# Optimization experiments

Measured on AMD Instinct MI355X. Metric: run time of the kernel, lower is better.

The kernel has to match this reference:

```python
import jax, jax.numpy as jnp
import numpy as np

D_MODEL = 512
D_STATE = 16
D_CONV = 4
EXPAND = 2
DT_RANK = 32
D_INNER = EXPAND * D_MODEL  # 1024


def setup_inputs() -> dict:
    key = jax.random.key(0)
    ks = jax.random.split(key, 8)
    s = 0.02
    return {
        "x": jax.random.normal(ks[0], (4, 2048, D_MODEL), jnp.float32),
        "ln1_w": jnp.ones((D_MODEL,), jnp.float32),
        "ln1_b": jnp.zeros((D_MODEL,), jnp.float32),
        "ln2_w": jnp.ones((D_MODEL,), jnp.float32),
        "ln2_b": jnp.zeros((D_MODEL,), jnp.float32),
        "W_in": jax.random.normal(ks[1], (D_MODEL, 2 * D_INNER), jnp.float32) * s,
        "conv_w": jax.random.normal(ks[2], (D_INNER, D_CONV), jnp.float32) * s,
        "conv_b": jnp.zeros((D_INNER,), jnp.float32),
        "W_xproj": jax.random.normal(ks[3], (D_INNER, DT_RANK + 2 * D_STATE), jnp.float32) * s,
        "W_dt": jax.random.normal(ks[4], (DT_RANK, D_INNER), jnp.float32) * s,
        "b_dt": jnp.full((D_INNER,), -4.6, jnp.float32),  # softplus(b_dt) ~ 0.01 init
        "A_log": jnp.log(jnp.broadcast_to(
            jnp.arange(1, D_STATE + 1, dtype=jnp.float32), (D_INNER, D_STATE))),
        "D_param": jnp.ones((D_INNER,), jnp.float32),
        "W_out": jax.random.normal(ks[5], (D_INNER, D_MODEL), jnp.float32) * s,
    }


def _layernorm(x, w, b, eps=1e-5):
    m = x.mean(-1, keepdims=True)
    v = ((x - m) ** 2).mean(-1, keepdims=True)
    return (x - m) / jnp.sqrt(v + eps) * w + b


def _selective_scan(x, W_in, conv_w, conv_b, W_xproj, W_dt, b_dt, A_log, D_param, W_out):
    B, L, _ = x.shape
    # input projection -> ssm branch u and gate branch z
    xz = x @ W_in                               # [B, L, 2E]
    u, z = jnp.split(xz, 2, axis=-1)            # each [B, L, E]

    # depthwise causal conv over L
    uc = jax.lax.conv_general_dilated(
        u.transpose(0, 2, 1),                   # [B, E, L]
        conv_w[:, None, :],                     # [E, 1, K]
        window_strides=(1,),
        padding=[(D_CONV - 1, 0)],
        dimension_numbers=("NCH", "OIH", "NCH"),
        feature_group_count=D_INNER,
    ).transpose(0, 2, 1)                        # [B, L, E]
    u = jax.nn.silu(uc + conv_b)

    # data-dependent SSM parameters
    x_dbl = u @ W_xproj                         # [B, L, R+2N]
    dt_r = x_dbl[..., :DT_RANK]
    Bm = x_dbl[..., DT_RANK:DT_RANK + D_STATE]  # [B, L, N]
    Cm = x_dbl[..., DT_RANK + D_STATE:]         # [B, L, N]
    dt = jax.nn.softplus(dt_r @ W_dt + b_dt)    # [B, L, E]
    A = -jnp.exp(A_log)                         # [E, N]

    def step(h, inp):
        dt_t, B_t, C_t, u_t = inp               # [B,E], [B,N], [B,N], [B,E]
        dA = jnp.exp(dt_t[:, :, None] * A)      # [B, E, N]
        h = dA * h + (dt_t * u_t)[:, :, None] * B_t[:, None, :]
        y = jnp.einsum("ben,bn->be", h, C_t)
        return h, y

    h0 = jnp.zeros((B, D_INNER, D_STATE), x.dtype)
    _, ys = jax.lax.scan(
        step, h0,
        (dt.transpose(1, 0, 2), Bm.transpose(1, 0, 2),
         Cm.transpose(1, 0, 2), u.transpose(1, 0, 2)))
    y = ys.transpose(1, 0, 2) + u * D_param     # skip via D
    y = y * jax.nn.silu(z)                      # gating
    return y @ W_out                            # [B, L, D]


def reference(x, ln1_w, ln1_b, ln2_w, ln2_b, W_in, conv_w, conv_b,
              W_xproj, W_dt, b_dt, A_log, D_param, W_out):
    residual = x
    h = _layernorm(x, ln1_w, ln1_b)
    h = _selective_scan(h, W_in, conv_w, conv_b, W_xproj, W_dt, b_dt,
                        A_log, D_param, W_out)
    return _layernorm(residual + h, ln2_w, ln2_b)
```

## Files before the change

kernel.cpp:

```cpp
#include <hip/hip_runtime.h>
#include <math.h>

#define BATCH   4
#define SEQ     2048
#define DMODEL  512
#define DINNER  1024
#define DSTATE  16
#define DCONV   4
#define DTRANK  32
#define ROWS    (BATCH*SEQ)

#define NCHUNK  128
#define CHUNK   (SEQ / NCHUNK)
#define NBE     (BATCH*DINNER)

typedef unsigned short u16;
typedef __attribute__((ext_vector_type(8))) u16 u16x8;
typedef __attribute__((ext_vector_type(4))) u16 u16x4;
typedef __attribute__((ext_vector_type(8))) short bf16x8;
typedef __attribute__((ext_vector_type(4))) float f32x4;
typedef __attribute__((ext_vector_type(2))) float f32x2;

__device__ inline float bf2f(u16 v) { return __uint_as_float(((unsigned)v) << 16); }
__device__ inline u16 f2bf(float f) {
    unsigned u = __float_as_uint(f);
    return (u16)((u + 0x7fff + ((u >> 16) & 1)) >> 16);
}
__device__ inline f32x2 fma2(f32x2 a, f32x2 b, f32x2 c) {
    return __builtin_elementwise_fma(a, b, c);
}


__global__ __launch_bounds__(256) void prep_weights(const float* __restrict__ W_in,
                                                    const float* __restrict__ W_out,
                                                    const float* __restrict__ W_xp,
                                                    const float* __restrict__ W_dt,
                                                    const float* __restrict__ cw,
                                                    const float* __restrict__ x,
                                                    const float* __restrict__ ln1_w,
                                                    const float* __restrict__ ln1_b,
                                                    u16* __restrict__ Wt,
                                                    u16* __restrict__ Wot,
                                                    u16* __restrict__ Wxt,
                                                    u16* __restrict__ Wdtt,
                                                    u16* __restrict__ cwT,
                                                    u16* __restrict__ hbf)
{
    const int t = blockIdx.x;
    if (t >= 1648) {
        __shared__ float ls[4], lq[4];
        const int row = (t - 1648) * 2 + (threadIdx.x >> 7);
        const int tid = threadIdx.x & 127;
        const int wv = threadIdx.x >> 6;
        float4 v = ((const float4*)(x + (size_t)row * DMODEL))[tid];
        float s = v.x + v.y + v.z + v.w;
        float q = v.x*v.x + v.y*v.y + v.z*v.z + v.w*v.w;
        #pragma unroll
        for (int o = 32; o > 0; o >>= 1) {
            s += __shfl_down(s, o);
            q += __shfl_down(q, o);
        }
        if ((threadIdx.x & 63) == 0) { ls[wv] = s; lq[wv] = q; }
        __syncthreads();
        const int rb = (threadIdx.x >> 7) * 2;
        float mean = (ls[rb] + ls[rb + 1]) * (1.f / DMODEL);
        float var  = (lq[rb] + lq[rb + 1]) * (1.f / DMODEL) - mean * mean;
        float inv  = rsqrtf(var + 1e-5f);
        float4 wv4 = ((const float4*)ln1_w)[tid];
        float4 bv = ((const float4*)ln1_b)[tid];
        u16x4 o4;
        o4.x = f2bf((v.x - mean) * inv * wv4.x + bv.x);
        o4.y = f2bf((v.y - mean) * inv * wv4.y + bv.y);
        o4.z = f2bf((v.z - mean) * inv * wv4.z + bv.z);
        o4.w = f2bf((v.w - mean) * inv * wv4.w + bv.w);
        ((u16x4*)(hbf + (size_t)row * DMODEL))[tid] = o4;
        return;
    }
    if (t >= 1632) {
        int idx = (t - 1632) * 256 + threadIdx.x;
        int j = idx >> 10, e = idx & (DINNER - 1);
        cwT[idx] = f2bf(cw[e * DCONV + j]);
        return;
    }
    const float* W; u16* Wo; int K, N, tl;
    if (t < 1024)      { W = W_in;  Wo = Wt;   K = 512;  N = 2048; tl = t; }
    else if (t < 1536) { W = W_out; Wo = Wot;  K = 1024; N = 512;  tl = t - 1024; }
    else if (t < 1600) { W = W_xp;  Wo = Wxt;  K = 1024; N = 64;   tl = t - 1536; }
    else               { W = W_dt;  Wo = Wdtt; K = 32;   N = 1024; tl = t - 1600; }
    const int ntx = N / 32;
    const int nb = (tl % ntx) * 32, kb = (tl / ntx) * 32;
    __shared__ float sh[32][33];
    const int xx = threadIdx.x & 31, yy = threadIdx.x >> 5;
    #pragma unroll
    for (int i = 0; i < 32; i += 8)
        sh[yy + i][xx] = W[(size_t)(kb + yy + i) * N + nb + xx];
    __syncthreads();
    #pragma unroll
    for (int i = 0; i < 32; i += 8)
        Wo[(size_t)(nb + yy + i) * K + kb + xx] = f2bf(sh[xx][yy + i]);
}

__global__ __launch_bounds__(128) void ln2_kernel(const float* __restrict__ x,
                                                  const u16* __restrict__ og,
                                                  const float* __restrict__ w,
                                                  const float* __restrict__ bb,
                                                  float* __restrict__ out)
{
    const int row = blockIdx.x;
    const int tid = threadIdx.x;
    float4 v = ((const float4*)(x + (size_t)row * DMODEL))[tid];
    u16x4 r4 = ((const u16x4*)(og + (size_t)row * DMODEL))[tid];
    v.x += bf2f(r4.x); v.y += bf2f(r4.y); v.z += bf2f(r4.z); v.w += bf2f(r4.w);
    float s = v.x + v.y + v.z + v.w;
    float q = v.x*v.x + v.y*v.y + v.z*v.z + v.w*v.w;
    #pragma unroll
    for (int o = 32; o > 0; o >>= 1) {
        s += __shfl_down(s, o);
        q += __shfl_down(q, o);
    }
    __shared__ float ls[2], lq[2];
    if ((tid & 63) == 0) { ls[tid >> 6] = s; lq[tid >> 6] = q; }
    __syncthreads();
    float mean = (ls[0] + ls[1]) * (1.f / DMODEL);
    float var  = (lq[0] + lq[1]) * (1.f / DMODEL) - mean * mean;
    float inv  = rsqrtf(var + 1e-5f);
    float4 wv = ((const float4*)w)[tid];
    float4 bv = ((const float4*)bb)[tid];
    float4 o4;
    o4.x = (v.x - mean) * inv * wv.x + bv.x;
    o4.y = (v.y - mean) * inv * wv.y + bv.y;
    o4.z = (v.z - mean) * inv * wv.z + bv.z;
    o4.w = (v.w - mean) * inv * wv.w + bv.w;
    ((float4*)(out + (size_t)row * DMODEL))[tid] = o4;
}

template<bool BF16OUT>
__global__ __launch_bounds__(256) void gemm_bf16(const u16* __restrict__ A, int lda,
                                                 const u16* __restrict__ Bt, int ldb,
                                                 void* __restrict__ Cout, int ldc, int K)
{
    __shared__ u16 Asm[128 * 32];
    __shared__ u16 Bsm[128 * 32];
    const int tid = threadIdx.x;
    const int wid = tid >> 6, lane = tid & 63;
    const int wm = wid >> 1, wn = wid & 1;
    const int bm = blockIdx.y * 128, bn = blockIdx.x * 128;

    f32x4 acc[4][4];
    #pragma unroll
    for (int m = 0; m < 4; ++m)
        #pragma unroll
        for (int n = 0; n < 4; ++n)
            acc[m][n] = (f32x4)(0.f);

    for (int k0 = 0; k0 < K; k0 += 32) {
        __syncthreads();
        #pragma unroll
        for (int j = 0; j < 2; ++j) {
            int c = (wid * 2 + j) * 64 + lane;
            int row = c >> 2, kp = (c & 3) << 3;
            const u16* ga = A  + (size_t)(bm + row) * lda + k0 + kp;
            const u16* gb = Bt + (size_t)(bn + row) * ldb + k0 + kp;
            __builtin_amdgcn_global_load_lds(
                (const __attribute__((address_space(1))) unsigned int*)ga,
                (__attribute__((address_space(3))) unsigned int*)(Asm + (wid * 2 + j) * 512),
                16, 0, 0);
            __builtin_amdgcn_global_load_lds(
                (const __attribute__((address_space(1))) unsigned int*)gb,
                (__attribute__((address_space(3))) unsigned int*)(Bsm + (wid * 2 + j) * 512),
                16, 0, 0);
        }
        __syncthreads();

        const int rl = lane & 15, kf = (lane >> 4) << 3;
        bf16x8 af[4], bfr[4];
        #pragma unroll
        for (int m = 0; m < 4; ++m)
            af[m] = *(const bf16x8*)&Asm[(wm * 64 + m * 16 + rl) * 32 + kf];
        #pragma unroll
        for (int n = 0; n < 4; ++n)
            bfr[n] = *(const bf16x8*)&Bsm[(wn * 64 + n * 16 + rl) * 32 + kf];
        #pragma unroll
        for (int m = 0; m < 4; ++m)
            #pragma unroll
            for (int n = 0; n < 4; ++n)
                acc[m][n] = __builtin_amdgcn_mfma_f32_16x16x32_bf16(af[m], bfr[n], acc[m][n], 0, 0, 0);
    }

    const int rl = lane & 15, rq = lane >> 4;
    #pragma unroll
    for (int m = 0; m < 4; ++m)
        #pragma unroll
        for (int n = 0; n < 4; ++n) {
            int r0 = bm + wm * 64 + m * 16 + rq * 4;
            int cc = bn + wn * 64 + n * 16 + rl;
            #pragma unroll
            for (int j = 0; j < 4; ++j) {
                if (BF16OUT)
                    ((u16*)Cout)[(size_t)(r0 + j) * ldc + cc] = f2bf(acc[m][n][j]);
                else
                    ((float*)Cout)[(size_t)(r0 + j) * ldc + cc] = acc[m][n][j];
            }
        }
}

__global__ __launch_bounds__(512) void conv_xproj_dt(const u16* __restrict__ xzb,
                                                     const u16* __restrict__ cwT,
                                                     const float* __restrict__ cb,
                                                     const u16* __restrict__ Wxt,
                                                     const u16* __restrict__ Wdtt,
                                                     const float* __restrict__ bdt,
                                                     u16* __restrict__ ucb,
                                                     float* __restrict__ xdbl,
                                                     u16* __restrict__ dty,
                                                     float* __restrict__ dts)
{
    __shared__ u16 uc_lds[16][1032];
    __shared__ float xd0[16][72];
    __shared__ float xd1[16][72];
    const int r16 = blockIdx.x;
    const int row0 = r16 * 16;
    const int cbch = ((r16 & 127) << 2) | (r16 >> 7);
    const int tid = threadIdx.x;
    const int lane = tid & 63, wid = tid >> 6;
    const int rl = lane & 15, hi = lane >> 4;

    #pragma unroll
    for (int i = 0; i < 4; ++i) {
        int task = tid + i * 512;
        int r = task >> 7;
        int e0 = (task & 127) * 8;
        int gr = row0 + r;
        int t = gr & (SEQ - 1);
        float4 cb0 = *(const float4*)&cb[e0];
        float4 cb1 = *(const float4*)&cb[e0 + 4];
        float acc[8] = {cb0.x, cb0.y, cb0.z, cb0.w, cb1.x, cb1.y, cb1.z, cb1.w};
        #pragma unroll
        for (int j = 0; j < 4; ++j) {
            int ts = t - 3 + j;
            if (ts >= 0) {
                u16x8 v = *(const u16x8*)&xzb[(size_t)(gr - 3 + j) * (2 * DINNER) + e0];
                u16x8 w = *(const u16x8*)&cwT[j * DINNER + e0];
                #pragma unroll
                for (int k = 0; k < 8; ++k)
                    acc[k] = fmaf(bf2f(v[k]), bf2f(w[k]), acc[k]);
            }
        }
        u16x8 o;
        #pragma unroll
        for (int k = 0; k < 8; ++k) {
            float sig = 1.f / (1.f + __expf(-acc[k]));
            o[k] = f2bf(acc[k] * sig);
        }
        *(u16x8*)&ucb[(size_t)gr * DINNER + e0] = o;
        *(u16x8*)&uc_lds[r][e0] = o;
    }
    __syncthreads();

    {
        const int tile = wid & 3, khalf = wid >> 2;
        f32x4 acc = (f32x4)(0.f);
        const int kbase = khalf * 512;
        #pragma unroll 4
        for (int kk = 0; kk < 512; kk += 32) {
            int k0 = kbase + kk;
            bf16x8 a = *(const bf16x8*)&uc_lds[rl][k0 + hi * 8];
            bf16x8 b = *(const bf16x8*)&Wxt[(size_t)(tile * 16 + rl) * DINNER + k0 + hi * 8];
            acc = __builtin_amdgcn_mfma_f32_16x16x32_bf16(a, b, acc, 0, 0, 0);
        }
        float (*dst)[72] = khalf ? xd1 : xd0;
        #pragma unroll
        for (int j = 0; j < 4; ++j)
            dst[hi * 4 + j][tile * 16 + rl] = acc[j];
    }
    __syncthreads();
    {
        int idx = tid * 2;
        #pragma unroll
        for (int i = 0; i < 2; ++i, ++idx) {
            int r = idx >> 6, c = idx & 63;
            float v = xd0[r][c] + xd1[r][c];
            xd0[r][c] = v;
            if (c >= DTRANK)
                xdbl[(size_t)(row0 + r) * 64 + c] = v;
        }
    }
    __syncthreads();

    {
        bf16x8 af;
        #pragma unroll
        for (int k = 0; k < 8; ++k)
            af[k] = (short)f2bf(xd0[rl][hi * 8 + k]);
        #pragma unroll
        for (int tile = 0; tile < 8; ++tile) {
            int cc = wid * 128 + tile * 16 + rl;
            bf16x8 bfr = *(const bf16x8*)&Wdtt[(size_t)cc * DTRANK + hi * 8];
            f32x4 acc = __builtin_amdgcn_mfma_f32_16x16x32_bf16(af, bfr, (f32x4)(0.f), 0, 0, 0);
            float bias = bdt[cc];
            float ssum = 0.f;
            #pragma unroll
            for (int j = 0; j < 4; ++j) {
                float v = acc[j] + bias;
                float sp = (v > 20.f) ? v : log1pf(__expf(v));
                u16 spb = f2bf(sp);
                dty[(size_t)(row0 + hi * 4 + j) * DINNER + cc] = spb;
                ssum += bf2f(spb);
            }
            ssum += __shfl_xor(ssum, 16);
            ssum += __shfl_xor(ssum, 32);
            if (hi == 0)
                dts[(size_t)cbch * DINNER + cc] = ssum;
        }
    }
}

__device__ inline void pow_tree16(float q, f32x2 dA2[8])
{
    float q2 = q * q;
    f32x2 q2s = {q2, q2};
    dA2[0] = (f32x2){q, q2};
    dA2[1] = dA2[0] * q2s;
    dA2[2] = dA2[1] * q2s;
    dA2[3] = dA2[2] * q2s;
    float q8 = dA2[3].y;
    f32x2 q8s = {q8, q8};
    dA2[4] = dA2[0] * q8s;
    dA2[5] = dA2[1] * q8s;
    dA2[6] = dA2[2] * q8s;
    dA2[7] = dA2[3] * q8s;
}

__global__ __launch_bounds__(256) void scan_pass1(const u16* __restrict__ dtb,
                                                  const u16* __restrict__ ucb,
                                                  const float* __restrict__ xdbl,
                                                  u16* __restrict__ hfinb)
{
    const int cb = blockIdx.x >> 2;
    const int e = ((blockIdx.x & 3) << 8) + threadIdx.x;
    const int b = cb & 3, c = cb >> 2;
    const int row0 = b * SEQ + c * CHUNK;

    __shared__ float bc[CHUNK][32];
    {
        int idx = threadIdx.x;
        #pragma unroll
        for (int i = 0; i < 2; ++i, idx += 256) {
            int r = idx >> 5, cix = idx & 31;
            bc[r][cix] = xdbl[(size_t)(row0 + r) * 64 + DTRANK + cix];
        }
    }
    __syncthreads();

    const u16* pdt = dtb + (size_t)row0 * DINNER + e;
    const u16* puc = ucb + (size_t)row0 * DINNER + e;

    f32x2 h2[8];
    #pragma unroll
    for (int k = 0; k < 8; ++k) h2[k] = (f32x2){0.f, 0.f};

    #pragma unroll 4
    for (int t = 0; t < CHUNK; ++t) {
        float dtv = bf2f(*pdt);
        float uv  = bf2f(*puc);
        float du  = dtv * uv;
        float q = __expf(-dtv);
        f32x2 dA2[8];
        pow_tree16(q, dA2);
        f32x2 du2 = {du, du};
        const f32x2* pbc = (const f32x2*)bc[t];
        #pragma unroll
        for (int k = 0; k < 8; ++k)
            h2[k] = fma2(dA2[k], h2[k], du2 * pbc[k]);
        pdt += DINNER; puc += DINNER;
    }
    #pragma unroll
    for (int k = 0; k < 8; ++k) {
        size_t si = (size_t)(cb * DSTATE + 2 * k) * DINNER + e;
        hfinb[si] = f2bf(h2[k].x);
        hfinb[si + DINNER] = f2bf(h2[k].y);
    }
}

__global__ __launch_bounds__(256) void scan_pass2(const float* __restrict__ dts,
                                                  u16* __restrict__ hfinb)
{
    int j = blockIdx.x * 256 + threadIdx.x;
    int e = j & (DINNER - 1);
    int n = (j >> 10) & 15;
    int b = j >> 14;
    const float mnp1 = -(float)(n + 1);
    float h = 0.f;
    #pragma unroll 4
    for (int c = 0; c < NCHUNK; ++c) {
        int cb = c * BATCH + b;
        size_t si = (size_t)(cb * DSTATE + n) * DINNER + e;
        float t = bf2f(hfinb[si]);
        hfinb[si] = f2bf(h);
        float P = __expf(mnp1 * dts[(size_t)cb * DINNER + e]);
        h = fmaf(P, h, t);
    }
}

__global__ __launch_bounds__(256) void scan_pass3(const u16* __restrict__ xzb,
                                                  const u16* __restrict__ ucb,
                                                  const float* __restrict__ xdbl,
                                                  const float* __restrict__ Dparam,
                                                  const u16* __restrict__ hinb,
                                                  u16* dty)
{
    const int cb = blockIdx.x >> 2;
    const int e = ((blockIdx.x & 3) << 8) + threadIdx.x;
    const int b = cb & 3, c = cb >> 2;
    const int row0 = b * SEQ + c * CHUNK;

    __shared__ float bc[CHUNK][32];
    {
        int idx = threadIdx.x;
        #pragma unroll
        for (int i = 0; i < 2; ++i, idx += 256) {
            int r = idx >> 5, cix = idx & 31;
            bc[r][cix] = xdbl[(size_t)(row0 + r) * 64 + DTRANK + cix];
        }
    }
    __syncthreads();

    const u16* pz  = xzb + (size_t)row0 * (2 * DINNER) + DINNER + e;
    const u16* puc = ucb + (size_t)row0 * DINNER + e;
    u16* pdty = dty + (size_t)row0 * DINNER + e;

    f32x2 h2[8];
    #pragma unroll
    for (int k = 0; k < 8; ++k) {
        size_t si = (size_t)(cb * DSTATE + 2 * k) * DINNER + e;
        h2[k] = (f32x2){bf2f(hinb[si]), bf2f(hinb[si + DINNER])};
    }
    const float Dv = Dparam[e];

    #pragma unroll 4
    for (int t = 0; t < CHUNK; ++t) {
        float dtv = bf2f(*pdty);
        float zv  = bf2f(*pz);
        float uv  = bf2f(*puc);
        float du  = dtv * uv;
        float q = __expf(-dtv);
        f32x2 dA2[8];
        pow_tree16(q, dA2);
        f32x2 du2 = {du, du};
        f32x2 acc = {0.f, 0.f};
        const f32x2* pbc = (const f32x2*)bc[t];
        #pragma unroll
        for (int k = 0; k < 8; ++k) {
            h2[k] = fma2(dA2[k], h2[k], du2 * pbc[k]);
            acc = fma2(h2[k], pbc[8 + k], acc);
        }
        float y = fmaf(uv, Dv, acc.x + acc.y);
        y *= zv / (1.f + __expf(-zv));
        *pdty = f2bf(y);
        pz += 2 * DINNER; puc += DINNER; pdty += DINNER;
    }
}

extern "C" void kernel_launch(void* const* d_in, const int* in_sizes, int n_in,
                              void* d_out, int out_size, void* d_ws, size_t ws_size,
                              hipStream_t stream)
{
    const float* x       = (const float*)d_in[0];
    const float* ln1_w   = (const float*)d_in[1];
    const float* ln1_b   = (const float*)d_in[2];
    const float* ln2_w   = (const float*)d_in[3];
    const float* ln2_b   = (const float*)d_in[4];
    const float* W_in    = (const float*)d_in[5];
    const float* conv_w  = (const float*)d_in[6];
    const float* conv_b  = (const float*)d_in[7];
    const float* W_xproj = (const float*)d_in[8];
    const float* W_dt    = (const float*)d_in[9];
    const float* b_dt    = (const float*)d_in[10];
    const float* D_param = (const float*)d_in[12];
    const float* W_out   = (const float*)d_in[13];
    float* out = (float*)d_out;
    float* ws  = (float*)d_ws;

    u16*   xzb   = (u16*)ws;
    u16*   ucb   = (u16*)(ws + 8388608);
    float* xdbl  = ws + 12582912;
    u16*   hbf   = (u16*)(ws + 13107200);
    u16*   Wt    = (u16*)(ws + 15204352);
    u16*   Wot   = (u16*)(ws + 15728640);
    u16*   dty   = (u16*)(ws + 15990784);
    float* dts   = ws + 20185088;
    u16*   hfinb = (u16*)(ws + 20709376);
    u16*   ogb   = (u16*)(ws + 24903680);
    u16*   Wxt   = (u16*)(ws + 27000832);
    u16*   cwT   = (u16*)(ws + 27033600);
    u16*   Wdtt  = (u16*)(ws + 27035648);

    prep_weights<<<1648 + ROWS / 2, 256, 0, stream>>>(W_in, W_out, W_xproj, W_dt,
                                                      conv_w, x, ln1_w, ln1_b,
                                                      Wt, Wot, Wxt, Wdtt, cwT, hbf);
    gemm_bf16<true><<<dim3(2048 / 128, ROWS / 128), 256, 0, stream>>>(hbf, 512, Wt, 512, xzb, 2048, 512);
    conv_xproj_dt<<<ROWS / 16, 512, 0, stream>>>(xzb, cwT, conv_b, Wxt, Wdtt, b_dt,
                                                 ucb, xdbl, dty, dts);
    scan_pass1<<<NBE * NCHUNK / 256, 256, 0, stream>>>(dty, ucb, xdbl, hfinb);
    scan_pass2<<<BATCH * DSTATE * DINNER / 256, 256, 0, stream>>>(dts, hfinb);
    scan_pass3<<<NBE * NCHUNK / 256, 256, 0, stream>>>(xzb, ucb, xdbl, D_param, hfinb, dty);
    gemm_bf16<true><<<dim3(512 / 128, ROWS / 128), 256, 0, stream>>>(dty, 1024, Wot, 1024, ogb, 512, 1024);
    ln2_kernel<<<ROWS, 128, 0, stream>>>(x, ogb, ln2_w, ln2_b, out);
}
```

Measured before the change: 183.8 us.

## Fuse chunked scan pass 1 into conv/xproj/dt kernel using LDS-resident tiles

Removes the separate scan_pass1 kernel and runs the per-chunk state accumulation at the end of conv_xproj_dt. The dt and conv outputs for the 16-row chunk stay in LDS, and B comes from the xd0 buffer. This saves one launch and the global re-read of dt, u and B. In exchange, each thread now carries two channels' 16-state recurrences serially, which raises register pressure and adds LDS use (a second 16x1032 buffer). That may lower occupancy of the fused kernel.

```diff
diff --git a/kernel.cpp b/kernel.cpp
--- a/kernel.cpp
+++ b/kernel.cpp
@@ -30,6 +30,22 @@
     return __builtin_elementwise_fma(a, b, c);
 }
 
+
+__device__ inline void pow_tree16(float q, f32x2 dA2[8])
+{
+    float q2 = q * q;
+    f32x2 q2s = {q2, q2};
+    dA2[0] = (f32x2){q, q2};
+    dA2[1] = dA2[0] * q2s;
+    dA2[2] = dA2[1] * q2s;
+    dA2[3] = dA2[2] * q2s;
+    float q8 = dA2[3].y;
+    f32x2 q8s = {q8, q8};
+    dA2[4] = dA2[0] * q8s;
+    dA2[5] = dA2[1] * q8s;
+    dA2[6] = dA2[2] * q8s;
+    dA2[7] = dA2[3] * q8s;
+}
 
 __global__ __launch_bounds__(256) void prep_weights(const float* __restrict__ W_in,
                                                     const float* __restrict__ W_out,
@@ -213,9 +229,11 @@
                                                      u16* __restrict__ ucb,
                                                      float* __restrict__ xdbl,
                                                      u16* __restrict__ dty,
-                                                     float* __restrict__ dts)
+                                                     float* __restrict__ dts,
+                                                     u16* __restrict__ hfinb)
 {
     __shared__ u16 uc_lds[16][1032];
+    __shared__ u16 dt_lds[16][1032];
     __shared__ float xd0[16][72];
     __shared__ float xd1[16][72];
     const int r16 = blockIdx.x;
@@ -305,6 +323,7 @@
                 float sp = (v > 20.f) ? v : log1pf(__expf(v));
                 u16 spb = f2bf(sp);
                 dty[(size_t)(row0 + hi * 4 + j) * DINNER + cc] = spb;
+                dt_lds[hi * 4 + j][cc] = spb;
                 ssum += bf2f(spb);
             }
             ssum += __shfl_xor(ssum, 16);
@@ -313,72 +332,45 @@
                 dts[(size_t)cbch * DINNER + cc] = ssum;
         }
     }
-}
-
-__device__ inline void pow_tree16(float q, f32x2 dA2[8])
-{
-    float q2 = q * q;
-    f32x2 q2s = {q2, q2};
-    dA2[0] = (f32x2){q, q2};
-    dA2[1] = dA2[0] * q2s;
-    dA2[2] = dA2[1] * q2s;
-    dA2[3] = dA2[2] * q2s;
-    float q8 = dA2[3].y;
-    f32x2 q8s = {q8, q8};
-    dA2[4] = dA2[0] * q8s;
-    dA2[5] = dA2[1] * q8s;
-    dA2[6] = dA2[2] * q8s;
-    dA2[7] = dA2[3] * q8s;
-}
-
-__global__ __launch_bounds__(256) void scan_pass1(const u16* __restrict__ dtb,
-                                                  const u16* __restrict__ ucb,
-                                                  const float* __restrict__ xdbl,
-                                                  u16* __restrict__ hfinb)
-{
-    const int cb = blockIdx.x >> 2;
-    const int e = ((blockIdx.x & 3) << 8) + threadIdx.x;
-    const int b = cb & 3, c = cb >> 2;
-    const int row0 = b * SEQ + c * CHUNK;
-
-    __shared__ float bc[CHUNK][32];
+    __syncthreads();
+
     {
-        int idx = threadIdx.x;
-        #pragma unroll
-        for (int i = 0; i < 2; ++i, idx += 256) {
-            int r = idx >> 5, cix = idx & 31;
-            bc[r][cix] = xdbl[(size_t)(row0 + r) * 64 + DTRANK + cix];
-        }
-    }
-    __syncthreads();
-
-    const u16* pdt = dtb + (size_t)row0 * DINNER + e;
-    const u16* puc = ucb + (size_t)row0 * DINNER + e;
-
-    f32x2 h2[8];
-    #pragma unroll
-    for (int k = 0; k < 8; ++k) h2[k] = (f32x2){0.f, 0.f};
-
-    #pragma unroll 4
-    for (int t = 0; t < CHUNK; ++t) {
-        float dtv = bf2f(*pdt);
-        float uv  = bf2f(*puc);
-        float du  = dtv * uv;
-        float q = __expf(-dtv);
-        f32x2 dA2[8];
-        pow_tree16(q, dA2);
-        f32x2 du2 = {du, du};
-        const f32x2* pbc = (const f32x2*)bc[t];
-        #pragma unroll
-        for (int k = 0; k < 8; ++k)
-            h2[k] = fma2(dA2[k], h2[k], du2 * pbc[k]);
-        pdt += DINNER; puc += DINNER;
-    }
-    #pragma unroll
-    for (int k = 0; k < 8; ++k) {
-        size_t si = (size_t)(cb * DSTATE + 2 * k) * DINNER + e;
-        hfinb[si] = f2bf(h2[k].x);
-        hfinb[si + DINNER] = f2bf(h2[k].y);
+        const int e1 = tid, e2 = tid + 512;
+        f32x2 hA[8], hB[8];
+        #pragma unroll
+        for (int k = 0; k < 8; ++k) { hA[k] = (f32x2){0.f, 0.f}; hB[k] = (f32x2){0.f, 0.f}; }
+        #pragma unroll 4
+        for (int t = 0; t < CHUNK; ++t) {
+            const f32x2* pbc = (const f32x2*)&xd0[t][DTRANK];
+            float dt1 = bf2f(dt_lds[t][e1]);
+            float uv1 = bf2f(uc_lds[t][e1]);
+            float du1 = dt1 * uv1;
+            float q1 = __expf(-dt1);
+            f32x2 dA1[8];
+            pow_tree16(q1, dA1);
+            f32x2 du1v = {du1, du1};
+            float dt2 = bf2f(dt_lds[t][e2]);
+            float uv2 = bf2f(uc_lds[t][e2]);
+            float du2 = dt2 * uv2;
+            float q2 = __expf(-dt2);
+            f32x2 dA2[8];
+            pow_tree16(q2, dA2);
+            f32x2 du2v = {du2, du2};
+            #pragma unroll
+            for (int k = 0; k < 8; ++k) {
+                f32x2 B = pbc[k];
+                hA[k] = fma2(dA1[k], hA[k], du1v * B);
+                hB[k] = fma2(dA2[k], hB[k], du2v * B);
+            }
+        }
+        #pragma unroll
+        for (int k = 0; k < 8; ++k) {
+            size_t si = (size_t)(cbch * DSTATE + 2 * k) * DINNER;
+            hfinb[si + e1] = f2bf(hA[k].x);
+            hfinb[si + DINNER + e1] = f2bf(hA[k].y);
+            hfinb[si + e2] = f2bf(hB[k].x);
+            hfinb[si + DINNER + e2] = f2bf(hB[k].y);
+        }
     }
 }
 
@@ -500,8 +492,7 @@
                                                       Wt, Wot, Wxt, Wdtt, cwT, hbf);
     gemm_bf16<true><<<dim3(2048 / 128, ROWS / 128), 256, 0, stream>>>(hbf, 512, Wt, 512, xzb, 2048, 512);
     conv_xproj_dt<<<ROWS / 16, 512, 0, stream>>>(xzb, cwT, conv_b, Wxt, Wdtt, b_dt,
-                                                 ucb, xdbl, dty, dts);
-    scan_pass1<<<NBE * NCHUNK / 256, 256, 0, stream>>>(dty, ucb, xdbl, hfinb);
+                                                 ucb, xdbl, dty, dts, hfinb);
     scan_pass2<<<BATCH * DSTATE * DINNER / 256, 256, 0, stream>>>(dts, hfinb);
     scan_pass3<<<NBE * NCHUNK / 256, 256, 0, stream>>>(xzb, ucb, xdbl, D_param, hfinb, dty);
     gemm_bf16<true><<<dim3(512 / 128, ROWS / 128), 256, 0, stream>>>(dty, 1024, Wot, 1024, ogb, 512, 1024);
```

Result: faster. 176.6 us, median of 2 (-3.9%).
